# Optimization experiments

Hardware: AMD Instinct MI355X
Metric: run time of the kernel (lower is better)

The kernel has to match this reference:

```python
import jax, jax.numpy as jnp
import numpy as np

HIDDEN = 512
REL = 16
N = 256
BSZ = 32


def setup_inputs() -> dict:
    key = jax.random.key(0)
    ks = jax.random.split(key, 8)
    columns = jax.random.normal(ks[0], (BSZ, N, HIDDEN), dtype=jnp.float32)
    logits = jax.random.normal(ks[1], (BSZ, N, 2), dtype=jnp.float32)
    adj = jax.random.randint(ks[2], (BSZ, N, N), 0, REL)
    # proj: Linear(2+hidden, hidden); stored as [in, out] so x @ W_proj + b_proj
    W_proj = jax.random.normal(ks[3], (2 + HIDDEN, HIDDEN), dtype=jnp.float32) / np.sqrt(2 + HIDDEN)
    b_proj = jnp.zeros((HIDDEN,), dtype=jnp.float32)
    ln_g = jnp.ones((HIDDEN,), dtype=jnp.float32)
    ln_b = jnp.zeros((HIDDEN,), dtype=jnp.float32)
    # low-rank relation weights: W [h,3,h], V [R,3] (xavier-ish)
    W = jax.random.normal(ks[4], (HIDDEN, 3, HIDDEN), dtype=jnp.float32) * np.sqrt(2.0 / (HIDDEN + HIDDEN))
    V = jax.random.normal(ks[5], (REL, 3), dtype=jnp.float32) * np.sqrt(2.0 / (REL + 3))
    return {"columns": columns, "logits": logits, "adj": adj,
            "W_proj": W_proj, "b_proj": b_proj, "ln_g": ln_g, "ln_b": ln_b,
            "W": W, "V": V}


def reference(columns, logits, adj, W_proj, b_proj, ln_g, ln_b, W, V):
    # proj + layernorm + gelu (dropout is identity in deterministic reference)
    h = jnp.concatenate([columns, logits], axis=-1) @ W_proj + b_proj  # [b,n,h]
    mu = jnp.mean(h, axis=-1, keepdims=True)
    var = jnp.mean(jnp.square(h - mu), axis=-1, keepdims=True)
    h = (h - mu) * jax.lax.rsqrt(var + 1e-5) * ln_g + ln_b
    x = jax.nn.gelu(h, approximate=False)  # torch nn.GELU default = exact erf

    R = V.shape[0]
    # low-rank relation weight mixing: Wr[r] = sum_t V[r,t] * W[:,t,:] -> [R,h,h]
    Wr = jnp.einsum('rt,hto->rho', V, W)

    # relation 0 uses identity adjacency (support = x); relations 1..R-1 use adj==r masks
    masks = (adj[..., None] == jnp.arange(1, R)).astype(x.dtype)  # [b,n,n,R-1]
    sup = jnp.einsum('bnmr,bmh->brnh', masks, x)                  # [b,R-1,n,h]

    out = jnp.einsum('bnh,ho->bno', x, Wr[0]) + jnp.einsum('brnh,rho->bno', sup, Wr[1:])
    return out
```

## Files before the change

kernel.cpp:

```cpp
#include <hip/hip_runtime.h>
#include <math.h>

#define HID 512
#define NSEQ 256
#define BSZ 32
#define ROWS (BSZ*NSEQ)
#define KP 576

typedef _Float16 half8_t __attribute__((ext_vector_type(8)));
typedef _Float16 half4_t __attribute__((ext_vector_type(4)));
typedef float f32x4 __attribute__((ext_vector_type(4)));

__device__ __forceinline__ void gload16(const _Float16* g, _Float16* l) {
    __builtin_amdgcn_global_load_lds(
        (const __attribute__((address_space(1))) unsigned int*)g,
        (__attribute__((address_space(3))) unsigned int*)l, 16, 0, 0);
}

__global__ __launch_bounds__(256) void prep(
    const float* __restrict__ cols, const float* __restrict__ logits,
    const float* __restrict__ Wp, const float* __restrict__ W,
    const int* __restrict__ adj, const float* __restrict__ V,
    _Float16* __restrict__ Acat, _Float16* __restrict__ WpT,
    _Float16* __restrict__ WcT, _Float16* __restrict__ C16b)
{
    __shared__ _Float16 ts[64][68];
    __shared__ float lut[16][3];
    __shared__ float V0s[3];
    const int blk = blockIdx.x, tid = threadIdx.x;

    if (blk < 1024) {
        int row0 = blk * 8;
        #pragma unroll
        for (int rr = 0; rr < 8; ++rr) {
            int row = row0 + rr;
            for (int k = tid; k < KP; k += 256) {
                float v = 0.f;
                if (k < 512) v = cols[(size_t)row*512 + k];
                else if (k < 514) v = logits[(size_t)row*2 + (k-512)];
                Acat[(size_t)row*KP + k] = (_Float16)v;
            }
        }
    } else if (blk < 1216) {
        int sub = blk - 1024;
        int c0 = (sub % 24) * 64, h0 = (sub / 24) * 64;
        int r = tid >> 2, q = tid & 3;
        #pragma unroll
        for (int i = 0; i < 4; ++i) {
            float4 v = *(const float4*)&W[(size_t)(h0+r)*1536 + c0 + q*16 + i*4];
            ts[r][q*16+i*4+0] = (_Float16)v.x;
            ts[r][q*16+i*4+1] = (_Float16)v.y;
            ts[r][q*16+i*4+2] = (_Float16)v.z;
            ts[r][q*16+i*4+3] = (_Float16)v.w;
        }
        __syncthreads();
        _Float16* op = WcT + (size_t)(c0 + r)*512 + h0 + q*16;
        #pragma unroll
        for (int i = 0; i < 4; ++i) {
            half4_t o;
            #pragma unroll
            for (int j = 0; j < 4; ++j) o[j] = ts[q*16+i*4+j][r];
            *(half4_t*)(op + i*4) = o;
        }
    } else if (blk < 1288) {
        int sub = blk - 1216;
        int k0 = (sub % 9) * 64, o0 = (sub / 9) * 64;
        int r = tid >> 2, q = tid & 3;
        int k = k0 + r;
        #pragma unroll
        for (int i = 0; i < 4; ++i) {
            float4 v = make_float4(0.f,0.f,0.f,0.f);
            if (k < 514) v = *(const float4*)&Wp[(size_t)k*HID + o0 + q*16 + i*4];
            ts[r][q*16+i*4+0] = (_Float16)v.x;
            ts[r][q*16+i*4+1] = (_Float16)v.y;
            ts[r][q*16+i*4+2] = (_Float16)v.z;
            ts[r][q*16+i*4+3] = (_Float16)v.w;
        }
        __syncthreads();
        _Float16* op = WpT + (size_t)(o0 + r)*KP + k0 + q*16;
        #pragma unroll
        for (int i = 0; i < 4; ++i) {
            half4_t o;
            #pragma unroll
            for (int j = 0; j < 4; ++j) o[j] = ts[q*16+i*4+j][r];
            *(half4_t*)(op + i*4) = o;
        }
    } else {
        if (tid < 48) { int r = tid/3, c = tid - r*3; lut[r][c] = (r >= 1) ? V[tid] : 0.f; }
        if (tid < 3) V0s[tid] = V[tid];
        __syncthreads();
        int sub = blk - 1288;
        int b = sub >> 2, nt = sub & 3;
        int n = nt*64 + (tid >> 2), mq = tid & 3;
        const int* ap = adj + ((size_t)(b*NSEQ + n))*NSEQ + mq*64;
        size_t ob = ((size_t)(b*NSEQ + n))*768 + mq*64;
        #pragma unroll
        for (int i = 0; i < 16; ++i) {
            int4 a4 = *(const int4*)(ap + i*4);
            int av[4] = { a4.x, a4.y, a4.z, a4.w };
            #pragma unroll
            for (int t = 0; t < 3; ++t) {
                half4_t o;
                #pragma unroll
                for (int j = 0; j < 4; ++j) {
                    int m = mq*64 + i*4 + j;
                    float v = lut[av[j]][t] + ((m == n) ? V0s[t] : 0.f);
                    o[j] = (_Float16)v;
                }
                *(half4_t*)(C16b + ob + (size_t)t*256 + i*4) = o;
            }
        }
    }
}

template<int KS, int NKT, int DEPTH, int NB, int NBLK, int EPI>
__global__ __launch_bounds__(512) void gemm512(
    const _Float16* __restrict__ A, const _Float16* __restrict__ Bm,
    const float* __restrict__ bias, void* __restrict__ outv)
{
    __shared__ _Float16 smem[DEPTH * 2 * 8192];
    _Float16* As = smem;
    _Float16* Bs = smem + DEPTH * 8192;
    const int tid = threadIdx.x;
    const int w = tid >> 6, lane = tid & 63;
    const int ell = blockIdx.x;
    const int s = (ell & 7) * (NB / 8) + (ell >> 3);
    const int row0 = (s / NBLK) * 128, col0 = (s % NBLK) * 128;
    const int wr = (w >> 2) * 64, wc = (w & 3) * 32;
    const _Float16* Ag = A + (size_t)row0 * KS;
    const _Float16* Bg = (EPI == 2)
        ? Bm + (size_t)(row0 >> 8) * 512 * KS + (size_t)col0 * KS
        : Bm + (size_t)col0 * KS;

    f32x4 acc[4][2] = {};

    auto stage = [&](int kt, int bi) {
        const _Float16* ga = Ag + kt * 64;
        const _Float16* gb = Bg + kt * 64;
        _Float16* la = As + bi * 8192;
        _Float16* lb = Bs + bi * 8192;
        #pragma unroll
        for (int l = 0; l < 2; ++l) {
            int gw = w * 128 + l * 64;
            int g  = gw + lane;
            int row = g >> 3;
            int c   = (g & 7) ^ (row & 7);
            gload16(ga + (size_t)row * KS + c * 8, la + gw * 8);
        }
        #pragma unroll
        for (int l = 0; l < 2; ++l) {
            int gw = w * 128 + l * 64;
            int g  = gw + lane;
            int row = g >> 3;
            int c   = (g & 7) ^ (row & 7);
            gload16(gb + (size_t)row * KS + c * 8, lb + gw * 8);
        }
    };

    auto compute = [&](int bi) {
        const _Float16* Ab = As + bi * 8192;
        const _Float16* Bb = Bs + bi * 8192;
        const int r16 = lane & 15;
        #pragma unroll
        for (int kh = 0; kh < 2; ++kh) {
            const int ks = (lane >> 4) + kh * 4;
            half8_t a[4], b[2];
            #pragma unroll
            for (int mi = 0; mi < 4; ++mi) {
                int row = wr + mi * 16 + r16;
                a[mi] = *(const half8_t*)(Ab + row * 64 + ((ks ^ (row & 7)) * 8));
            }
            #pragma unroll
            for (int ni = 0; ni < 2; ++ni) {
                int col = wc + ni * 16 + r16;
                b[ni] = *(const half8_t*)(Bb + col * 64 + ((ks ^ (col & 7)) * 8));
            }
            #pragma unroll
            for (int mi = 0; mi < 4; ++mi)
                #pragma unroll
                for (int ni = 0; ni < 2; ++ni)
                    acc[mi][ni] = __builtin_amdgcn_mfma_f32_16x16x32_f16(
                        a[mi], b[ni], acc[mi][ni], 0, 0, 0);
        }
    };

    #pragma unroll
    for (int i = 0; i < DEPTH; ++i) stage(i, i);

    int buf = 0;
    #pragma unroll 1
    for (int kt = 0; kt < NKT - (DEPTH - 1); ++kt) {
        if constexpr (DEPTH == 2) asm volatile("s_waitcnt vmcnt(4)" ::: "memory");
        else                      asm volatile("s_waitcnt vmcnt(8)" ::: "memory");
        __builtin_amdgcn_s_barrier();
        __builtin_amdgcn_s_setprio(1);
        compute(buf);
        __builtin_amdgcn_s_setprio(0);
        asm volatile("" ::: "memory");
        __builtin_amdgcn_s_barrier();
        if (kt + DEPTH < NKT) stage(kt + DEPTH, buf);
        ++buf; if (buf == DEPTH) buf = 0;
    }
    if constexpr (DEPTH == 3) {
        asm volatile("s_waitcnt vmcnt(4)" ::: "memory");
        __builtin_amdgcn_s_barrier();
        __builtin_amdgcn_s_setprio(1);
        compute(buf);
        __builtin_amdgcn_s_setprio(0);
        asm volatile("" ::: "memory");
        __builtin_amdgcn_s_barrier();
        ++buf; if (buf == DEPTH) buf = 0;
    }
    asm volatile("s_waitcnt vmcnt(0)" ::: "memory");
    __builtin_amdgcn_s_barrier();
    compute(buf);

    if constexpr (EPI == 0 || EPI == 2) {
        float* out = (float*)outv;
        #pragma unroll
        for (int mi = 0; mi < 4; ++mi) {
            int r = row0 + wr + mi * 16 + (lane >> 4) * 4;
            #pragma unroll
            for (int ni = 0; ni < 2; ++ni) {
                int cidx = col0 + wc + ni * 16 + (lane & 15);
                float bv = (EPI == 0) ? bias[cidx] : 0.f;
                #pragma unroll
                for (int q = 0; q < 4; ++q)
                    out[(size_t)(r + q) * HID + cidx] = acc[mi][ni][q] + bv;
            }
        }
    } else {
        __syncthreads();
        _Float16* ep = smem;
        #pragma unroll
        for (int mi = 0; mi < 4; ++mi) {
            int rb = wr + mi * 16 + (lane >> 4) * 4;
            #pragma unroll
            for (int ni = 0; ni < 2; ++ni) {
                int c = wc + ni * 16 + (lane & 15);
                half4_t h4;
                #pragma unroll
                for (int q = 0; q < 4; ++q) h4[q] = (_Float16)acc[mi][ni][q];
                *(half4_t*)&ep[c * 136 + rb] = h4;
            }
        }
        __syncthreads();
        const int b = row0 >> 8, m0 = row0 & 255, t = col0 >> 9, o0 = col0 & 511;
        _Float16* yb = (_Float16*)outv + ((size_t)b * 512 + o0) * 768 + (size_t)t * 256 + m0;
        #pragma unroll
        for (int it = 0; it < 4; ++it) {
            int g = it * 512 + tid;
            int c = g >> 4, m8 = g & 15;
            *(half8_t*)(yb + (size_t)c * 768 + m8 * 8) =
                *(const half8_t*)&ep[c * 136 + m8 * 8];
        }
    }
}

__global__ __launch_bounds__(256) void ln_gelu_f16(const float* __restrict__ h,
    const float* __restrict__ g, const float* __restrict__ bb,
    _Float16* __restrict__ xrm)
{
    int row = blockIdx.x;
    int tid = threadIdx.x;
    float v0 = h[row*512 + tid];
    float v1 = h[row*512 + 256 + tid];
    __shared__ float red[4];
    int wid = tid >> 6, lane = tid & 63;

    float s = v0 + v1;
    #pragma unroll
    for (int off = 32; off; off >>= 1) s += __shfl_down(s, off);
    if (lane == 0) red[wid] = s;
    __syncthreads();
    float mu = (red[0]+red[1]+red[2]+red[3]) * (1.f/512.f);
    __syncthreads();

    float d0 = v0 - mu, d1 = v1 - mu;
    float q = d0*d0 + d1*d1;
    #pragma unroll
    for (int off = 32; off; off >>= 1) q += __shfl_down(q, off);
    if (lane == 0) red[wid] = q;
    __syncthreads();
    float var = (red[0]+red[1]+red[2]+red[3]) * (1.f/512.f);
    float rs = rsqrtf(var + 1e-5f);

    float y0 = d0*rs*g[tid] + bb[tid];
    float y1 = d1*rs*g[tid+256] + bb[tid+256];
    y0 = 0.5f*y0*(1.f + erff(y0*0.70710678118654752f));
    y1 = 0.5f*y1*(1.f + erff(y1*0.70710678118654752f));
    xrm[(size_t)row*512 + tid]       = (_Float16)y0;
    xrm[(size_t)row*512 + 256 + tid] = (_Float16)y1;
}

extern "C" void kernel_launch(void* const* d_in, const int* in_sizes, int n_in,
                              void* d_out, int out_size, void* d_ws, size_t ws_size,
                              hipStream_t stream)
{
    const float* cols   = (const float*)d_in[0];
    const float* logits = (const float*)d_in[1];
    const int*   adj    = (const int*)  d_in[2];
    const float* Wp     = (const float*)d_in[3];
    const float* bp     = (const float*)d_in[4];
    const float* lg     = (const float*)d_in[5];
    const float* lb     = (const float*)d_in[6];
    const float* W      = (const float*)d_in[7];
    const float* V      = (const float*)d_in[8];
    float* out  = (float*)d_out;

    float* xbuf = (float*)d_ws;
    char* p = (char*)d_ws + (size_t)ROWS*HID*4;
    _Float16* Acat = (_Float16*)p;  p += (size_t)ROWS*KP*2;
    _Float16* WpT  = (_Float16*)p;  p += (size_t)HID*KP*2;
    _Float16* WcT  = (_Float16*)p;  p += (size_t)1536*HID*2;
    _Float16* C16b = (_Float16*)p;  p += (size_t)ROWS*768*2;
    _Float16* YTb  = (_Float16*)p;  p += (size_t)BSZ*HID*768*2;
    _Float16* Xrm  = Acat;

    prep<<<1416, 256, 0, stream>>>(cols, logits, Wp, W, adj, V, Acat, WpT, WcT, C16b);
    gemm512<KP, 9, 3, 256, 4, 0><<<256, 512, 0, stream>>>(Acat, WpT, bp, xbuf);
    ln_gelu_f16<<<ROWS, 256, 0, stream>>>(xbuf, lg, lb, Xrm);
    gemm512<512, 8, 2, 768, 12, 1><<<768, 512, 0, stream>>>(Xrm, WcT, nullptr, YTb);
    gemm512<768, 12, 3, 256, 4, 2><<<256, 512, 0, stream>>>(C16b, YTb, nullptr, out);
}
```

Measured before the change: 78.36 us.

## Store projection output in fp16 and coalesce adjacency coefficient prep

The projection GEMM epilogue now stages results through shared memory and writes an fp16 row-major buffer with 16-byte stores, replacing scattered fp32 stores. LayerNorm+GELU then reads and writes that buffer in place. Together these halve the bytes moving between the projection and the normalisation step. The adjacency-to-coefficient prep is also reorganised so each wavefront reads a full contiguous adjacency row, and it uses an fp16 lookup table. The trade-off is an extra fp16 rounding of the pre-LayerNorm activations.

```diff
diff --git a/kernel.cpp b/kernel.cpp
--- a/kernel.cpp
+++ b/kernel.cpp
@@ -25,8 +25,8 @@
     _Float16* __restrict__ WcT, _Float16* __restrict__ C16b)
 {
     __shared__ _Float16 ts[64][68];
-    __shared__ float lut[16][3];
-    __shared__ float V0s[3];
+    __shared__ _Float16 lutH[48];
+    __shared__ _Float16 V0h[3];
     const int blk = blockIdx.x, tid = threadIdx.x;
 
     if (blk < 1024) {
@@ -86,28 +86,25 @@
             *(half4_t*)(op + i*4) = o;
         }
     } else {
-        if (tid < 48) { int r = tid/3, c = tid - r*3; lut[r][c] = (r >= 1) ? V[tid] : 0.f; }
-        if (tid < 3) V0s[tid] = V[tid];
+        if (tid < 48) { int r = tid/3; lutH[tid] = (_Float16)((r >= 1) ? V[tid] : 0.f); }
+        if (tid < 3) V0h[tid] = (_Float16)V[tid];
         __syncthreads();
         int sub = blk - 1288;
         int b = sub >> 2, nt = sub & 3;
-        int n = nt*64 + (tid >> 2), mq = tid & 3;
-        const int* ap = adj + ((size_t)(b*NSEQ + n))*NSEQ + mq*64;
-        size_t ob = ((size_t)(b*NSEQ + n))*768 + mq*64;
+        int w = tid >> 6, lane = tid & 63;
         #pragma unroll
         for (int i = 0; i < 16; ++i) {
-            int4 a4 = *(const int4*)(ap + i*4);
+            int n = nt*64 + w*16 + i;
+            int4 a4 = *(const int4*)(adj + ((size_t)(b*NSEQ + n))*NSEQ + lane*4);
             int av[4] = { a4.x, a4.y, a4.z, a4.w };
+            size_t ob = ((size_t)(b*NSEQ + n))*768 + lane*4;
             #pragma unroll
             for (int t = 0; t < 3; ++t) {
                 half4_t o;
                 #pragma unroll
-                for (int j = 0; j < 4; ++j) {
-                    int m = mq*64 + i*4 + j;
-                    float v = lut[av[j]][t] + ((m == n) ? V0s[t] : 0.f);
-                    o[j] = (_Float16)v;
-                }
-                *(half4_t*)(C16b + ob + (size_t)t*256 + i*4) = o;
+                for (int j = 0; j < 4; ++j) o[j] = lutH[av[j]*3 + t];
+                if ((n >> 2) == lane) o[n & 3] = (_Float16)(o[n & 3] + V0h[t]);
+                *(half4_t*)(C16b + ob + (size_t)t*256) = o;
             }
         }
     }
@@ -215,7 +212,7 @@
     __builtin_amdgcn_s_barrier();
     compute(buf);
 
-    if constexpr (EPI == 0 || EPI == 2) {
+    if constexpr (EPI == 2) {
         float* out = (float*)outv;
         #pragma unroll
         for (int mi = 0; mi < 4; ++mi) {
@@ -223,11 +220,34 @@
             #pragma unroll
             for (int ni = 0; ni < 2; ++ni) {
                 int cidx = col0 + wc + ni * 16 + (lane & 15);
-                float bv = (EPI == 0) ? bias[cidx] : 0.f;
                 #pragma unroll
                 for (int q = 0; q < 4; ++q)
-                    out[(size_t)(r + q) * HID + cidx] = acc[mi][ni][q] + bv;
-            }
+                    out[(size_t)(r + q) * HID + cidx] = acc[mi][ni][q];
+            }
+        }
+    } else if constexpr (EPI == 0) {
+        __syncthreads();
+        _Float16* ep = smem;
+        #pragma unroll
+        for (int mi = 0; mi < 4; ++mi) {
+            int rb = wr + mi * 16 + (lane >> 4) * 4;
+            #pragma unroll
+            for (int ni = 0; ni < 2; ++ni) {
+                int c = wc + ni * 16 + (lane & 15);
+                float bv = bias[col0 + c];
+                #pragma unroll
+                for (int q = 0; q < 4; ++q)
+                    ep[(rb + q) * 136 + c] = (_Float16)(acc[mi][ni][q] + bv);
+            }
+        }
+        __syncthreads();
+        _Float16* ob = (_Float16*)outv + (size_t)row0 * HID + col0;
+        #pragma unroll
+        for (int it = 0; it < 4; ++it) {
+            int g = it * 512 + tid;
+            int r = g >> 4, c8 = g & 15;
+            *(half8_t*)(ob + (size_t)r * HID + c8 * 8) =
+                *(const half8_t*)&ep[r * 136 + c8 * 8];
         }
     } else {
         __syncthreads();
@@ -257,14 +277,13 @@
     }
 }
 
-__global__ __launch_bounds__(256) void ln_gelu_f16(const float* __restrict__ h,
-    const float* __restrict__ g, const float* __restrict__ bb,
-    _Float16* __restrict__ xrm)
+__global__ __launch_bounds__(256) void ln_gelu_ip(_Float16* __restrict__ h,
+    const float* __restrict__ g, const float* __restrict__ bb)
 {
     int row = blockIdx.x;
     int tid = threadIdx.x;
-    float v0 = h[row*512 + tid];
-    float v1 = h[row*512 + 256 + tid];
+    float v0 = (float)h[(size_t)row*512 + tid];
+    float v1 = (float)h[(size_t)row*512 + 256 + tid];
     __shared__ float red[4];
     int wid = tid >> 6, lane = tid & 63;
 
@@ -289,8 +308,8 @@
     float y1 = d1*rs*g[tid+256] + bb[tid+256];
     y0 = 0.5f*y0*(1.f + erff(y0*0.70710678118654752f));
     y1 = 0.5f*y1*(1.f + erff(y1*0.70710678118654752f));
-    xrm[(size_t)row*512 + tid]       = (_Float16)y0;
-    xrm[(size_t)row*512 + 256 + tid] = (_Float16)y1;
+    h[(size_t)row*512 + tid]       = (_Float16)y0;
+    h[(size_t)row*512 + 256 + tid] = (_Float16)y1;
 }
 
 extern "C" void kernel_launch(void* const* d_in, const int* in_sizes, int n_in,
@@ -308,18 +327,17 @@
     const float* V      = (const float*)d_in[8];
     float* out  = (float*)d_out;
 
-    float* xbuf = (float*)d_ws;
-    char* p = (char*)d_ws + (size_t)ROWS*HID*4;
+    char* p = (char*)d_ws;
+    _Float16* Xh   = (_Float16*)p;  p += (size_t)ROWS*HID*2;
     _Float16* Acat = (_Float16*)p;  p += (size_t)ROWS*KP*2;
     _Float16* WpT  = (_Float16*)p;  p += (size_t)HID*KP*2;
     _Float16* WcT  = (_Float16*)p;  p += (size_t)1536*HID*2;
     _Float16* C16b = (_Float16*)p;  p += (size_t)ROWS*768*2;
     _Float16* YTb  = (_Float16*)p;  p += (size_t)BSZ*HID*768*2;
-    _Float16* Xrm  = Acat;
 
     prep<<<1416, 256, 0, stream>>>(cols, logits, Wp, W, adj, V, Acat, WpT, WcT, C16b);
-    gemm512<KP, 9, 3, 256, 4, 0><<<256, 512, 0, stream>>>(Acat, WpT, bp, xbuf);
-    ln_gelu_f16<<<ROWS, 256, 0, stream>>>(xbuf, lg, lb, Xrm);
-    gemm512<512, 8, 2, 768, 12, 1><<<768, 512, 0, stream>>>(Xrm, WcT, nullptr, YTb);
+    gemm512<KP, 9, 3, 256, 4, 0><<<256, 512, 0, stream>>>(Acat, WpT, bp, Xh);
+    ln_gelu_ip<<<ROWS, 256, 0, stream>>>(Xh, lg, lb);
+    gemm512<512, 8, 2, 768, 12, 1><<<768, 512, 0, stream>>>(Xh, WcT, nullptr, YTb);
     gemm512<768, 12, 3, 256, 4, 2><<<256, 512, 0, stream>>>(C16b, YTb, nullptr, out);
 }
```

After: 67.87 us. 1.15x faster.
